# Kernel optimization log

Measured on AMD Instinct MI355X. Metric: run time of the kernel, lower is better.

The kernel has to match this reference:

```python
import jax, jax.numpy as jnp
import numpy as np

NEG_SLOPE = 0.2
K_L = 0.5
K_G = 0.5
TEMP_G = 1e-3


def _leaky(v):
    return jnp.where(v >= 0, v, NEG_SLOPE * v)


def _topk_row_mask(scores, keep):
    # scores: [n, n, h]; torch.topk(dim=0) -> indices [keep, n] per head,
    # then head_mask[indices, :] = 1 selects whole ROWS (any column hit).
    n = scores.shape[0]
    s = jnp.transpose(scores, (1, 2, 0))        # [n_cols, h, n_rows]
    _, idx = jax.lax.top_k(s, keep)             # [n_cols, h, keep]

    def per_head(idx_h):                        # idx_h: [n_cols, keep]
        return jnp.zeros((n,), scores.dtype).at[idx_h.reshape(-1)].set(1.0)

    rows = jax.vmap(per_head, in_axes=1, out_axes=0)(idx)  # [h, n_rows]
    return jnp.transpose(rows)[:, None, :]      # [n_rows, 1, h] broadcast over cols


def setup_inputs() -> dict:
    key = jax.random.key(0)
    ks = jax.random.split(key, 8)
    n, in_f, feat_dim = 1024, 256, 128
    H, F = 4, 64                                # n_heads, n_hidden (out_features=256)
    feats = jax.random.normal(ks[0], (n, feat_dim), dtype=jnp.float32)
    x = jax.random.normal(ks[1], (n, in_f), dtype=jnp.float32)
    adj = jax.random.randint(ks[2], (n, n, 1), 0, 2).astype(jnp.int32)
    sc = 0.05
    W_l = jax.random.normal(ks[3], (in_f, H * F), dtype=jnp.float32) * sc
    W_r = jax.random.normal(ks[4], (in_f, H * F), dtype=jnp.float32) * sc
    attn_w = jax.random.normal(ks[5], (F,), dtype=jnp.float32) * sc
    W_delta = jax.random.normal(ks[6], (2 * F, F), dtype=jnp.float32) * sc
    b_delta = jnp.zeros((F,), dtype=jnp.float32)
    return {"feats": feats, "x": x, "adj": adj, "W_l": W_l, "W_r": W_r,
            "attn_w": attn_w, "W_delta": W_delta, "b_delta": b_delta}


def reference(feats, x, adj, W_l, W_r, attn_w, W_delta, b_delta):
    n = x.shape[0]
    F = attn_w.shape[0]
    H = W_l.shape[1] // F
    g_l = (x @ W_l).reshape(n, H, F)
    g_r = (x @ W_r).reshape(n, H, F)
    # g_sum[i, j] = g_l[j] + g_r[i]  (repeat vs repeat_interleave ordering)
    g_sum = g_r[:, None, :, :] + g_l[None, :, :, :]          # [n, n, H, F]
    e = jnp.einsum('ijhf,f->ijh', _leaky(g_sum), attn_w)     # [n, n, H]

    mask_adj = adj > 0                                        # [n, n, 1]
    a_l = jax.nn.softmax(jnp.where(mask_adj, e, -jnp.inf), axis=1)
    a_1nd = a_l * mask_adj.astype(e.dtype)

    keep_l = int(n * (1.0 - K_L))
    a_filt = a_1nd * _topk_row_mask(a_1nd, keep_l)
    attn_local = jnp.einsum('ijh,jhf->ihf', a_filt, g_r)     # [n, H, F]

    omega = jax.nn.softmax(e, axis=1)
    fn = (feats - feats.min(axis=0)) / (feats.max(axis=0) - feats.min(axis=0))
    fn = jnp.where(jnp.isnan(fn), 0.0, fn)
    g_rn = (g_r - g_r.min(axis=0)) / (g_r.max(axis=0) - g_r.min(axis=0))
    nf = jnp.linalg.norm(fn, axis=1)                          # [n] (index j)
    ng = jnp.linalg.norm(g_rn, axis=2)                        # [n, H] (index i)
    alpha = jax.nn.softmax(jnp.abs(nf[None, :, None] - ng[:, None, :]), axis=1)
    gamma = 0.5 * (omega + (1.0 - alpha))

    keep_g = int(n * (1.0 - K_G))
    gf = gamma * _topk_row_mask(gamma, keep_g)
    gf = jax.nn.softmax(jnp.where(gf == 0, 1e-10, gf) / TEMP_G, axis=1)
    attn_global = jnp.einsum('ijh,jhf->ihf', gf, g_r)         # [n, H, F]

    inter = _leaky(jnp.concatenate([attn_local, attn_global], axis=2) @ W_delta + b_delta)
    delta = jax.nn.softmax(inter, axis=1)                     # softmax over heads (torch dim=1)
    attn_res = delta * attn_local + (1.0 - delta) * attn_global
    return attn_res.reshape(n, H * F)
```

## Files before the change

### kernel.cpp

```cpp
#include <hip/hip_runtime.h>
#include <cstdint>
#include <cstddef>

#define N 1024
#define HN 4
#define FDIM 64
#define KSEL 512
#define FLT_MAX_ 3.402823466e+38f

__device__ __forceinline__ float wred_sum(float v){
#pragma unroll
  for(int o=32;o>0;o>>=1) v += __shfl_down(v,o,64);
  return v;
}
__device__ __forceinline__ float bfly_sum(float v){
#pragma unroll
  for(int o=1;o<64;o<<=1) v += __shfl_xor(v,o,64);
  return v;
}
__device__ __forceinline__ float bfly_max(float v){
#pragma unroll
  for(int o=1;o<64;o<<=1) v = fmaxf(v,__shfl_xor(v,o,64));
  return v;
}
__device__ __forceinline__ int bfly_sumi(int v){
#pragma unroll
  for(int o=1;o<64;o<<=1) v += __shfl_xor(v,o,64);
  return v;
}
__device__ __forceinline__ float bred_sum(float v, float* scr){
  int t=threadIdx.x;
  v = wred_sum(v);
  __syncthreads();
  if((t&63)==0) scr[t>>6]=v;
  __syncthreads();
  return (scr[0]+scr[1])+(scr[2]+scr[3]);
}

__global__ __launch_bounds__(256) void stage1(const float* __restrict__ x,
                                              const float* __restrict__ W_l,
                                              const float* __restrict__ W_r,
                                              const int* __restrict__ adj,
                                              const float* __restrict__ feats,
                                              float* __restrict__ g_l,
                                              float* __restrict__ g_r,
                                              unsigned* __restrict__ adjbit,
                                              int* __restrict__ masks,
                                              float* __restrict__ pmin_f,
                                              float* __restrict__ pmax_f){
  int bx = blockIdx.x, t = threadIdx.x;
  if(bx < 512){
    const float* __restrict__ W = (bx >= 256) ? W_r : W_l;
    float* __restrict__ g = (bx >= 256) ? g_r : g_l;
    int i0 = (bx & 255)*4;
    float acc[4] = {0.f,0.f,0.f,0.f};
#pragma unroll 8
    for(int k=0;k<256;k++){
      float w = W[(size_t)k*256 + t];
#pragma unroll
      for(int r=0;r<4;r++) acc[r] = fmaf(x[(size_t)(i0+r)*256 + k], w, acc[r]);
    }
#pragma unroll
    for(int r=0;r<4;r++) g[(size_t)(i0+r)*256 + t] = acc[r];
  } else if(bx < 1536){
    int i = bx - 512, w = t>>6, lane = t&63;
    if(i < 32) masks[i*256 + t] = 0;
#pragma unroll
    for(int it=0; it<4; it++){
      int j = w*256 + it*64 + lane;
      int v = adj[(size_t)i*N + j];
      unsigned long long mb = __ballot(v > 0);
      if(lane == 0){
        adjbit[i*32 + w*8 + it*2]     = (unsigned)mb;
        adjbit[i*32 + w*8 + it*2 + 1] = (unsigned)(mb >> 32);
      }
    }
  } else {
    int chunk = bx - 1536;
    if(t < 128){
      float lo = FLT_MAX_, hi = -FLT_MAX_;
      int r0 = chunk*64;
      for(int r=0;r<64;r++){
        float v = feats[(size_t)(r0+r)*128 + t];
        lo = fminf(lo,v); hi = fmaxf(hi,v);
      }
      pmin_f[chunk*128+t]=lo; pmax_f[chunk*128+t]=hi;
    }
  }
}

__global__ __launch_bounds__(256) void stage2(const float* __restrict__ g_l,
                                              const float* __restrict__ g_r,
                                              const float* __restrict__ attn_w,
                                              const float* __restrict__ feats,
                                              const float* __restrict__ pmin_f, const float* __restrict__ pmax_f,
                                              float* __restrict__ pmin_g, float* __restrict__ pmax_g,
                                              float* __restrict__ nf,
                                              float* __restrict__ e){
  __shared__ __align__(16) float smem[2*64*68 + 128];
  int bx = blockIdx.x, t = threadIdx.x;
  if(bx < 1024){
    float* grs = smem;
    float* gls = smem + 64*68;
    float* aw  = smem + 2*64*68;
    float* aw2 = aw + 64;
    int h = bx >> 8, i0 = ((bx>>4)&15)*64, j0 = (bx&15)*64;
    if(t < 64){ float w = attn_w[t]; aw[t]=w; aw2[t]=0.2f*w; }
#pragma unroll
    for(int k=0;k<16;k++){
      int idx = t + k*256; int r = idx>>6, f = idx&63;
      grs[r*68+f] = g_r[(size_t)(i0+r)*256 + h*64 + f];
      gls[r*68+f] = g_l[(size_t)(j0+r)*256 + h*64 + f];
    }
    __syncthreads();
    int tj = t&15, ti = t>>4;
    float acc[4][4];
#pragma unroll
    for(int a=0;a<4;a++)
#pragma unroll
      for(int b=0;b<4;b++) acc[a][b]=0.f;
    for(int fc=0; fc<64; fc+=4){
      float4 wv  = *(float4*)&aw[fc];
      float4 wv2 = *(float4*)&aw2[fc];
      float4 ga4[4], gb4[4];
#pragma unroll
      for(int a=0;a<4;a++) ga4[a] = *(float4*)&grs[(ti*4+a)*68+fc];
#pragma unroll
      for(int b=0;b<4;b++) gb4[b] = *(float4*)&gls[(tj+16*b)*68+fc];
#pragma unroll
      for(int a=0;a<4;a++)
#pragma unroll
        for(int b=0;b<4;b++){
          float s0 = ga4[a].x + gb4[b].x;
          float s1 = ga4[a].y + gb4[b].y;
          float s2 = ga4[a].z + gb4[b].z;
          float s3 = ga4[a].w + gb4[b].w;
          acc[a][b] = fmaf(s0, (s0>=0.f)?wv.x:wv2.x, acc[a][b]);
          acc[a][b] = fmaf(s1, (s1>=0.f)?wv.y:wv2.y, acc[a][b]);
          acc[a][b] = fmaf(s2, (s2>=0.f)?wv.z:wv2.z, acc[a][b]);
          acc[a][b] = fmaf(s3, (s3>=0.f)?wv.w:wv2.w, acc[a][b]);
        }
    }
#pragma unroll
    for(int a=0;a<4;a++)
#pragma unroll
      for(int b=0;b<4;b++){
        int i = i0 + ti*4 + a, j = j0 + tj + 16*b;
        e[((size_t)h*N + i)*N + j] = acc[a][b];
      }
  } else if(bx < 1040){
    int chunk = bx - 1024;
    float lo = FLT_MAX_, hi = -FLT_MAX_;
    int r0 = chunk*64;
    for(int r=0;r<64;r++){
      float v = g_r[(size_t)(r0+r)*256 + t];
      lo = fminf(lo,v); hi = fmaxf(hi,v);
    }
    pmin_g[chunk*256+t]=lo; pmax_g[chunk*256+t]=hi;
  } else {
    int i = bx - 1040;
    float* scr = smem;
    float u = 0.f;
    if(t < 128){
      float lo = FLT_MAX_, hi = -FLT_MAX_;
#pragma unroll
      for(int k=0;k<16;k++){
        lo = fminf(lo, pmin_f[k*128+t]);
        hi = fmaxf(hi, pmax_f[k*128+t]);
      }
      float d = hi - lo;
      float v = feats[(size_t)i*128 + t];
      u = (d==0.f) ? 0.f : (v - lo)/d;
    }
    float tot = bred_sum(u*u, scr);
    if(t==0) nf[i] = sqrtf(tot);
  }
}

__global__ __launch_bounds__(256) void row_stats(const float* __restrict__ e,
                                                 const unsigned* __restrict__ adjbit,
                                                 const float* __restrict__ nf,
                                                 const float* __restrict__ g_r,
                                                 const float* __restrict__ pmin_g, const float* __restrict__ pmax_g,
                                                 float* __restrict__ ng,
                                                 float* __restrict__ mlA, float* __restrict__ islA,
                                                 float* __restrict__ moA, float* __restrict__ isoA,
                                                 float* __restrict__ maA, float* __restrict__ isaA,
                                                 float* __restrict__ mgA, float* __restrict__ sgA){
  int i = blockIdx.x, t = threadIdx.x, h = t>>6, lane = t&63;
  float glo = FLT_MAX_, ghi = -FLT_MAX_;
#pragma unroll
  for(int k=0;k<16;k++){
    glo = fminf(glo, pmin_g[k*256 + h*64 + lane]);
    ghi = fmaxf(ghi, pmax_g[k*256 + h*64 + lane]);
  }
  float dg = ghi - glo;
  float ug = (g_r[(size_t)i*256 + h*64 + lane] - glo)/dg;
  float ngv = sqrtf(bfly_sum(ug*ug));
  if(lane==0) ng[h*N + i] = ngv;

  size_t base = ((size_t)h*N + i)*N;
  float er[16], nfr[16];
  unsigned nib[4];
#pragma unroll
  for(int c=0;c<4;c++){
    float4 e4 = *(const float4*)(e  + base + c*256 + lane*4);
    float4 n4 = *(const float4*)(nf + c*256 + lane*4);
    er[c*4+0]=e4.x; er[c*4+1]=e4.y; er[c*4+2]=e4.z; er[c*4+3]=e4.w;
    nfr[c*4+0]=n4.x; nfr[c*4+1]=n4.y; nfr[c*4+2]=n4.z; nfr[c*4+3]=n4.w;
    nib[c] = (adjbit[i*32 + c*8 + (lane>>3)] >> ((lane&7)*4)) & 0xFu;
  }
  float ml=-FLT_MAX_, mo=-FLT_MAX_, ma=-FLT_MAX_;
#pragma unroll
  for(int c=0;c<4;c++)
#pragma unroll
    for(int k=0;k<4;k++){
      int q = c*4+k;
      float ev = er[q];
      mo = fmaxf(mo, ev);
      if((nib[c]>>k)&1) ml = fmaxf(ml, ev);
      ma = fmaxf(ma, fabsf(nfr[q]-ngv));
    }
  ml = bfly_max(ml); mo = bfly_max(mo); ma = bfly_max(ma);
  float sl=0.f, so=0.f, sa=0.f;
#pragma unroll
  for(int c=0;c<4;c++)
#pragma unroll
    for(int k=0;k<4;k++){
      int q = c*4+k;
      float ev = er[q];
      so += __expf(ev-mo);
      if((nib[c]>>k)&1) sl += __expf(ev-ml);
      sa += __expf(fabsf(nfr[q]-ngv)-ma);
    }
  sl = bfly_sum(sl); so = bfly_sum(so); sa = bfly_sum(sa);
  float isl = 1.f/sl, iso = 1.f/so, isa = 1.f/sa;
  float gg[16];
  float mg = -FLT_MAX_;
#pragma unroll
  for(int q=0;q<16;q++){
    float ev = er[q];
    float omega = __expf(ev-mo)*iso;
    float alpha = __expf(fabsf(nfr[q]-ngv)-ma)*isa;
    float g = 0.5f*(omega + 1.f - alpha);
    gg[q] = g;
    mg = fmaxf(mg, g);
  }
  mg = bfly_max(mg);
  float sg = 0.f;
#pragma unroll
  for(int q=0;q<16;q++) sg += __expf((gg[q]-mg)/1e-3f);
  sg = bfly_sum(sg);
  if(lane==0){
    mlA[h*N+i]=ml; islA[h*N+i]=isl;
    moA[h*N+i]=mo; isoA[h*N+i]=iso;
    maA[h*N+i]=ma; isaA[h*N+i]=isa;
    mgA[h*N+i]=mg; sgA[h*N+i]=sg;
  }
}

__global__ __launch_bounds__(256) void applyT(float* __restrict__ e,
                                              float* __restrict__ gamT,
                                              const unsigned* __restrict__ adjbit,
                                              const float* __restrict__ nf,
                                              const float* __restrict__ mlA, const float* __restrict__ islA,
                                              const float* __restrict__ moA, const float* __restrict__ isoA,
                                              const float* __restrict__ maA, const float* __restrict__ isaA,
                                              const float* __restrict__ ng){
  __shared__ __align__(16) float buf1[64][65];
  __shared__ __align__(16) float buf2[64][65];
  __shared__ __align__(16) float buf3[64][65];
  __shared__ float rml[64], risl[64], rmo[64], riso[64], rma[64], risa[64], rng[64], nfs[64];
  int h = blockIdx.y;
  int pp = blockIdx.x; int a = 0;
  while(pp >= 16 - a){ pp -= 16 - a; a++; }
  int b = a + pp;
  int t = threadIdx.x;
  int rg = t >> 4, c4 = t & 15;

  int i0 = a*64, j0 = b*64;
  if(t < 64){
    int o = h*N + i0 + t;
    rml[t]=mlA[o]; risl[t]=islA[o]; rmo[t]=moA[o]; riso[t]=isoA[o];
    rma[t]=maA[o]; risa[t]=isaA[o]; rng[t]=ng[o]; nfs[t]=nf[j0+t];
  }
  __syncthreads();
  float4 ev[4]; unsigned nb[4];
#pragma unroll
  for(int k=0;k<4;k++){
    int row = rg*4+k;
    ev[k] = *(const float4*)(e + ((size_t)h*N + i0+row)*N + j0 + c4*4);
    nb[k] = (adjbit[(size_t)(i0+row)*32 + (j0>>5) + (c4>>3)] >> ((c4&7)*4)) & 0xFu;
  }
#pragma unroll
  for(int k=0;k<4;k++){
    int row = rg*4+k;
    float ml=rml[row], isl=risl[row], mo=rmo[row], iso=riso[row];
    float ma=rma[row], isa=risa[row], ngv=rng[row];
    float evc[4] = {ev[k].x,ev[k].y,ev[k].z,ev[k].w};
#pragma unroll
    for(int c=0;c<4;c++){
      int j = c4*4+c;
      buf2[j][row] = ((nb[k]>>c)&1) ? __expf(evc[c]-ml)*isl : 0.f;
      float omega = __expf(evc[c]-mo)*iso;
      float alpha = __expf(fabsf(nfs[j]-ngv)-ma)*isa;
      buf1[j][row] = 0.5f*(omega + 1.f - alpha);
    }
  }
  __syncthreads();
#pragma unroll
  for(int k=0;k<4;k++){
    int jr = rg*4+k;
    *(float4*)(gamT + ((size_t)h*N + j0+jr)*N + i0 + c4*4) = *(float4*)&buf1[jr][c4*4];
  }
  if(a == b){
#pragma unroll
    for(int k=0;k<4;k++){
      int jr = rg*4+k;
      *(float4*)(e + ((size_t)h*N + j0+jr)*N + i0 + c4*4) = *(float4*)&buf2[jr][c4*4];
    }
    return;
  }
  int i1 = b*64, j1 = a*64;
  __syncthreads();
  if(t < 64){
    int o = h*N + i1 + t;
    rml[t]=mlA[o]; risl[t]=islA[o]; rmo[t]=moA[o]; riso[t]=isoA[o];
    rma[t]=maA[o]; risa[t]=isaA[o]; rng[t]=ng[o]; nfs[t]=nf[j1+t];
  }
#pragma unroll
  for(int k=0;k<4;k++){
    int row = rg*4+k;
    ev[k] = *(const float4*)(e + ((size_t)h*N + i1+row)*N + j1 + c4*4);
    nb[k] = (adjbit[(size_t)(i1+row)*32 + (j1>>5) + (c4>>3)] >> ((c4&7)*4)) & 0xFu;
  }
  __syncthreads();
#pragma unroll
  for(int k=0;k<4;k++){
    int jr = rg*4+k;
    *(float4*)(e + ((size_t)h*N + i1+jr)*N + j1 + c4*4) = *(float4*)&buf2[jr][c4*4];
  }
#pragma unroll
  for(int k=0;k<4;k++){
    int row = rg*4+k;
    float ml=rml[row], isl=risl[row], mo=rmo[row], iso=riso[row];
    float ma=rma[row], isa=risa[row], ngv=rng[row];
    float evc[4] = {ev[k].x,ev[k].y,ev[k].z,ev[k].w};
#pragma unroll
    for(int c=0;c<4;c++){
      int j = c4*4+c;
      buf3[j][row] = ((nb[k]>>c)&1) ? __expf(evc[c]-ml)*isl : 0.f;
      float omega = __expf(evc[c]-mo)*iso;
      float alpha = __expf(fabsf(nfs[j]-ngv)-ma)*isa;
      buf1[j][row] = 0.5f*(omega + 1.f - alpha);
    }
  }
  __syncthreads();
#pragma unroll
  for(int k=0;k<4;k++){
    int jr = rg*4+k;
    *(float4*)(gamT + ((size_t)h*N + j1+jr)*N + i1 + c4*4) = *(float4*)&buf1[jr][c4*4];
    *(float4*)(e    + ((size_t)h*N + j1+jr)*N + i1 + c4*4) = *(float4*)&buf3[jr][c4*4];
  }
}

__global__ __launch_bounds__(256) void colselect6(const float* __restrict__ a1T,
                                                  const float* __restrict__ gaT,
                                                  int* __restrict__ mask_l,
                                                  int* __restrict__ mask_g){
  __shared__ __align__(16) int hist[4][256];
  int t = threadIdx.x, w = t>>6, lane = t&63;
  int gcol = blockIdx.x*4 + w;
  int z  = gcol >> 12;
  int hj = gcol & 4095;
  int h  = hj >> 10;
  const float* __restrict__ src = (z ? gaT : a1T) + (size_t)hj * (size_t)N;
  int* __restrict__ mask = z ? mask_g : mask_l;
  int* hw = hist[w];

  unsigned ur[16];
#pragma unroll
  for(int c=0;c<4;c++){
    uint4 u4 = ((const uint4*)src)[c*64 + lane];
    ur[c*4+0]=u4.x; ur[c*4+1]=u4.y; ur[c*4+2]=u4.z; ur[c*4+3]=u4.w;
  }
  int np = 0;
#pragma unroll
  for(int q=0;q<16;q++) np += (ur[q] != 0u) ? 1 : 0;
  int cnt_pos = bfly_sumi(np);

  unsigned T; int tneed; int tiecnt = -1;
  if(cnt_pos < KSEL){
    T = 0u; tneed = KSEL - cnt_pos;
  } else {
    unsigned prefix = 0; int kth = KSEL;
#pragma unroll
    for(int b=3;b>=0;b--){
      *(int4*)&hw[lane*4] = make_int4(0,0,0,0);
#pragma unroll
      for(int q=0;q<16;q++){
        unsigned u = ur[q];
        bool act = (b==3) || ((u >> (8*(b+1))) == prefix);
        if(act){
          int bucket = (u >> (8*b)) & 0xFF;
          unsigned long long mball = __ballot(true);
          int lead = __ffsll(mball) - 1;
          int maj = __shfl(bucket, lead, 64);
          if(bucket == maj){
            int cnt = (int)__popcll(__ballot(true));
            if(lane == lead) atomicAdd(&hw[maj], cnt);
          } else {
            atomicAdd(&hw[bucket], 1);
          }
        }
      }
      int4 hv = *(int4*)&hw[lane*4];
      int s = hv.x+hv.y+hv.z+hv.w;
      int P = s;
#pragma unroll
      for(int off=1; off<64; off<<=1){
        int q2 = __shfl_up(P, off, 64);
        if(lane >= off) P += q2;
      }
      int total = __shfl(P, 63, 64);
      int suffChunk  = total - (P - s);
      int suffChunkN = total - P;
      bool cross = (suffChunk >= kth) && (suffChunkN < kth);
      int selb=0, newk=0, tcnt=0;
      if(cross){
        int s3 = suffChunkN + hv.w;
        int s2 = s3 + hv.z;
        int s1 = s2 + hv.y;
        if(s3 >= kth){ selb=4*lane+3; newk = kth - suffChunkN; tcnt=hv.w; }
        else if(s2 >= kth){ selb=4*lane+2; newk = kth - s3; tcnt=hv.z; }
        else if(s1 >= kth){ selb=4*lane+1; newk = kth - s2; tcnt=hv.y; }
        else { selb=4*lane; newk = kth - s1; tcnt=hv.x; }
      }
      unsigned long long cm = __ballot(cross);
      int csrc = __ffsll(cm) - 1;
      selb   = __shfl(selb, csrc, 64);
      kth    = __shfl(newk, csrc, 64);
      tiecnt = __shfl(tcnt, csrc, 64);
      prefix = (prefix << 8) | (unsigned)selb;
    }
    T = prefix; tneed = kth;
  }

  if(tiecnt == tneed){
#pragma unroll
    for(int c=0;c<4;c++)
#pragma unroll
      for(int k2=0;k2<4;k2++){
        int i = c*256 + lane*4 + k2;
        if(ur[c*4+k2] >= T) mask[h*N + i] = 1;
      }
  } else {
    int base = 0;
#pragma unroll
    for(int c=0;c<4;c++){
      int tc=0;
#pragma unroll
      for(int k2=0;k2<4;k2++) tc += (ur[c*4+k2]==T)?1:0;
      int pc = tc;
#pragma unroll
      for(int off=1; off<64; off<<=1){
        int q2 = __shfl_up(pc, off, 64);
        if(lane >= off) pc += q2;
      }
      int ctot = __shfl(pc, 63, 64);
      int run = base + pc - tc;
#pragma unroll
      for(int k2=0;k2<4;k2++){
        int i = c*256 + lane*4 + k2;
        unsigned u = ur[c*4+k2];
        bool sel = (u > T) || (u == T && run < tneed);
        run += (u==T)?1:0;
        if(sel) mask[h*N + i] = 1;
      }
      base += ctot;
    }
  }
}

__global__ __launch_bounds__(256) void attn_mm(const float* __restrict__ a1T,
                                               const float* __restrict__ gaT,
                                               const float* __restrict__ g_r,
                                               const float* __restrict__ mgA,
                                               const float* __restrict__ sgA,
                                               const int* __restrict__ mask_g,
                                               float* __restrict__ partL,
                                               float* __restrict__ partG){
  __shared__ __align__(16) float a_t[32][36];
  __shared__ __align__(16) float p_t[32][36];
  __shared__ __align__(16) float b_s[32][68];
  __shared__ float mgv[32], isgv[32];
  __shared__ int mgf[32];
  int i0 = blockIdx.x*32, h = blockIdx.y, s = blockIdx.z, j0 = s*128;
  int t = threadIdx.x;
  if(t < 32){
    mgv[t]  = mgA[h*N + i0 + t];
    isgv[t] = 1.f / sgA[h*N + i0 + t];
    mgf[t]  = mask_g[h*N + i0 + t];
  }
  __syncthreads();
  int fq = t & 15, iq = t >> 4;
  float4 accL[2], accG[2];
#pragma unroll
  for(int r=0;r<2;r++){ accL[r]=make_float4(0,0,0,0); accG[r]=make_float4(0,0,0,0); }
  for(int sub=0; sub<4; sub++){
    int jb = j0 + sub*32;
    {
      int jj = t>>3, i4 = t&7;
      size_t base = ((size_t)h*N + jb + jj)*N + i0 + i4*4;
      *(float4*)&a_t[jj][i4*4] = *(const float4*)(a1T + base);
      float4 g4 = *(const float4*)(gaT + base);
      int ii = i4*4;
      const float inv = 1.f/1024.f;
      float4 p4;
      p4.x = mgf[ii+0] ? __expf((g4.x - mgv[ii+0])/1e-3f)*isgv[ii+0] : inv;
      p4.y = mgf[ii+1] ? __expf((g4.y - mgv[ii+1])/1e-3f)*isgv[ii+1] : inv;
      p4.z = mgf[ii+2] ? __expf((g4.z - mgv[ii+2])/1e-3f)*isgv[ii+2] : inv;
      p4.w = mgf[ii+3] ? __expf((g4.w - mgv[ii+3])/1e-3f)*isgv[ii+3] : inv;
      *(float4*)&p_t[jj][i4*4] = p4;
#pragma unroll
      for(int k=0;k<2;k++){
        int idx = t + k*256;
        int jb2 = idx>>4, d4 = idx&15;
        *(float4*)&b_s[jb2][d4*4] = *(const float4*)(g_r + (size_t)(jb+jb2)*256 + h*64 + d4*4);
      }
    }
    __syncthreads();
#pragma unroll 8
    for(int j=0;j<32;j++){
      float4 bv = *(float4*)&b_s[j][fq*4];
      float2 av = *(float2*)&a_t[j][iq*2];
      float2 pv = *(float2*)&p_t[j][iq*2];
      accL[0].x = fmaf(av.x, bv.x, accL[0].x); accL[0].y = fmaf(av.x, bv.y, accL[0].y);
      accL[0].z = fmaf(av.x, bv.z, accL[0].z); accL[0].w = fmaf(av.x, bv.w, accL[0].w);
      accL[1].x = fmaf(av.y, bv.x, accL[1].x); accL[1].y = fmaf(av.y, bv.y, accL[1].y);
      accL[1].z = fmaf(av.y, bv.z, accL[1].z); accL[1].w = fmaf(av.y, bv.w, accL[1].w);
      accG[0].x = fmaf(pv.x, bv.x, accG[0].x); accG[0].y = fmaf(pv.x, bv.y, accG[0].y);
      accG[0].z = fmaf(pv.x, bv.z, accG[0].z); accG[0].w = fmaf(pv.x, bv.w, accG[0].w);
      accG[1].x = fmaf(pv.y, bv.x, accG[1].x); accG[1].y = fmaf(pv.y, bv.y, accG[1].y);
      accG[1].z = fmaf(pv.y, bv.z, accG[1].z); accG[1].w = fmaf(pv.y, bv.w, accG[1].w);
    }
    __syncthreads();
  }
#pragma unroll
  for(int r=0;r<2;r++){
    int i = i0 + iq*2 + r;
    size_t o = ((size_t)s*N + i)*256 + h*64 + fq*4;
    *(float4*)&partL[o] = accL[r];
    *(float4*)&partG[o] = accG[r];
  }
}

__global__ __launch_bounds__(256) void epilogue(const float* __restrict__ partL,
                                                const float* __restrict__ partG,
                                                const int* __restrict__ mask_l,
                                                const float* __restrict__ W_delta,
                                                const float* __restrict__ b_delta,
                                                float* __restrict__ out){
  __shared__ float cat[4][128];
  __shared__ float inter_s[4][64];
  int i = blockIdx.x, t = threadIdx.x;
  int h = t>>6, f = t&63;
  float sl = 0.f, sg = 0.f;
#pragma unroll
  for(int s2=0;s2<8;s2++){
    size_t o = ((size_t)s2*N + i)*256 + h*64 + f;
    sl += partL[o];
    sg += partG[o];
  }
  if(!mask_l[h*N + i]) sl = 0.f;
  cat[h][f]      = sl;
  cat[h][64 + f] = sg;
  __syncthreads();
  float d = b_delta[f];
  for(int c=0;c<128;c++) d = fmaf(cat[h][c], W_delta[(size_t)c*64 + f], d);
  d = (d >= 0.f) ? d : 0.2f*d;
  inter_s[h][f] = d;
  __syncthreads();
  float m = inter_s[0][f];
#pragma unroll
  for(int hh=1;hh<4;hh++) m = fmaxf(m, inter_s[hh][f]);
  float ssum = 0.f;
#pragma unroll
  for(int hh=0;hh<4;hh++) ssum += __expf(inter_s[hh][f]-m);
  float delta = __expf(d - m)/ssum;
  out[(size_t)i*256 + h*64 + f] = delta*sl + (1.f - delta)*sg;
}

extern "C" void kernel_launch(void* const* d_in, const int* in_sizes, int n_in,
                              void* d_out, int out_size, void* d_ws, size_t ws_size,
                              hipStream_t stream) {
  const float* feats  = (const float*)d_in[0];
  const float* x      = (const float*)d_in[1];
  const int*   adj    = (const int*)  d_in[2];
  const float* W_l    = (const float*)d_in[3];
  const float* W_r    = (const float*)d_in[4];
  const float* attn_w = (const float*)d_in[5];
  const float* W_delta= (const float*)d_in[6];
  const float* b_delta= (const float*)d_in[7];
  float* out = (float*)d_out;

  float* ws = (float*)d_ws;
  size_t off = 0;
  float* g_l   = ws+off; off += (size_t)N*256;
  float* g_r   = ws+off; off += (size_t)N*256;
  float* e     = ws+off; off += (size_t)HN*N*N;
  float* gam   = ws+off; off += (size_t)HN*N*N;
  float* partL = ws+off; off += (size_t)8*N*256;
  float* partG = ws+off; off += (size_t)8*N*256;
  float* pmin_f= ws+off; off += 16*128;
  float* pmax_f= ws+off; off += 16*128;
  float* pmin_g= ws+off; off += 16*256;
  float* pmax_g= ws+off; off += 16*256;
  float* nf    = ws+off; off += N;
  float* ng    = ws+off; off += (size_t)HN*N;
  float* mlA   = ws+off; off += (size_t)HN*N;
  float* islA  = ws+off; off += (size_t)HN*N;
  float* moA   = ws+off; off += (size_t)HN*N;
  float* isoA  = ws+off; off += (size_t)HN*N;
  float* maA   = ws+off; off += (size_t)HN*N;
  float* isaA  = ws+off; off += (size_t)HN*N;
  float* mgA   = ws+off; off += (size_t)HN*N;
  float* sgA   = ws+off; off += (size_t)HN*N;
  int* mask_l  = (int*)(ws+off); off += (size_t)HN*N;
  int* mask_g  = (int*)(ws+off); off += (size_t)HN*N;
  unsigned* adjbit = (unsigned*)(ws+off); off += (size_t)N*32;

  stage1<<<1552, 256, 0, stream>>>(x, W_l, W_r, adj, feats, g_l, g_r, adjbit, mask_l, pmin_f, pmax_f);

  stage2<<<2064, 256, 0, stream>>>(g_l, g_r, attn_w, feats, pmin_f, pmax_f,
                                   pmin_g, pmax_g, nf, e);

  row_stats<<<N, 256, 0, stream>>>(e, adjbit, nf, g_r, pmin_g, pmax_g, ng,
                                   mlA, islA, moA, isoA, maA, isaA, mgA, sgA);

  applyT<<<dim3(136,HN), 256, 0, stream>>>(e, gam, adjbit, nf, mlA, islA, moA, isoA, maA, isaA, ng);

  colselect6<<<2048, 256, 0, stream>>>(e, gam, mask_l, mask_g);

  attn_mm<<<dim3(32,HN,8), 256, 0, stream>>>(e, gam, g_r, mgA, sgA, mask_g, partL, partG);

  epilogue<<<N, 256, 0, stream>>>(partL, partG, mask_l, W_delta, b_delta, out);
}
```

Before: 195.2 us.

## Double-buffer attn_mm LDS tiles and widen block tile to 64 rows

The attn_mm kernel now tiles 64 output rows per block instead of 32, so each thread accumulates a 4x4 register tile rather than 2x4, which halves the grid. Shared-memory tiles are double-buffered: global loads for the next 32-column chunk go into registers while the current chunk is computed, then are written to the other buffer. The aim is to hide global load latency and raise FMA work per LDS read. The cost is more registers and shared memory per block and fewer blocks (512) to spread across CUs.

```diff
diff --git a/kernel.cpp b/kernel.cpp
--- a/kernel.cpp
+++ b/kernel.cpp
@@ -490,65 +490,106 @@
                                                const int* __restrict__ mask_g,
                                                float* __restrict__ partL,
                                                float* __restrict__ partG){
-  __shared__ __align__(16) float a_t[32][36];
-  __shared__ __align__(16) float p_t[32][36];
-  __shared__ __align__(16) float b_s[32][68];
-  __shared__ float mgv[32], isgv[32];
-  __shared__ int mgf[32];
-  int i0 = blockIdx.x*32, h = blockIdx.y, s = blockIdx.z, j0 = s*128;
+  __shared__ __align__(16) float a_t[2][32][68];
+  __shared__ __align__(16) float p_t[2][32][68];
+  __shared__ __align__(16) float b_s[2][32][68];
+  __shared__ float mgv[64], isgv[64];
+  __shared__ int mgf[64];
+  int i0 = blockIdx.x*64, h = blockIdx.y, s = blockIdx.z, j0 = s*128;
   int t = threadIdx.x;
-  if(t < 32){
+  if(t < 64){
     mgv[t]  = mgA[h*N + i0 + t];
     isgv[t] = 1.f / sgA[h*N + i0 + t];
     mgf[t]  = mask_g[h*N + i0 + t];
   }
-  __syncthreads();
   int fq = t & 15, iq = t >> 4;
-  float4 accL[2], accG[2];
-#pragma unroll
-  for(int r=0;r<2;r++){ accL[r]=make_float4(0,0,0,0); accG[r]=make_float4(0,0,0,0); }
-  for(int sub=0; sub<4; sub++){
-    int jb = j0 + sub*32;
-    {
-      int jj = t>>3, i4 = t&7;
-      size_t base = ((size_t)h*N + jb + jj)*N + i0 + i4*4;
-      *(float4*)&a_t[jj][i4*4] = *(const float4*)(a1T + base);
-      float4 g4 = *(const float4*)(gaT + base);
-      int ii = i4*4;
-      const float inv = 1.f/1024.f;
-      float4 p4;
+  int ju0 = t>>4,        i40 = t&15;
+  int ju1 = (t+256)>>4,  i41 = t&15;
+
+  float4 va[2], vg[2], vb[2];
+  {
+    int jb = j0;
+    size_t b0 = ((size_t)h*N + jb + ju0)*N + i0 + i40*4;
+    size_t b1 = ((size_t)h*N + jb + ju1)*N + i0 + i41*4;
+    va[0] = *(const float4*)(a1T + b0);  va[1] = *(const float4*)(a1T + b1);
+    vg[0] = *(const float4*)(gaT + b0);  vg[1] = *(const float4*)(gaT + b1);
+    vb[0] = *(const float4*)(g_r + (size_t)(jb+ju0)*256 + h*64 + i40*4);
+    vb[1] = *(const float4*)(g_r + (size_t)(jb+ju1)*256 + h*64 + i41*4);
+  }
+  __syncthreads();
+  {
+    const float inv = 1.f/1024.f;
+#pragma unroll
+    for(int k=0;k<2;k++){
+      int ju = k ? ju1 : ju0, ii = (k ? i41 : i40)*4;
+      *(float4*)&a_t[0][ju][(k?i41:i40)*4] = va[k];
+      float4 g4 = vg[k], p4;
       p4.x = mgf[ii+0] ? __expf((g4.x - mgv[ii+0])/1e-3f)*isgv[ii+0] : inv;
       p4.y = mgf[ii+1] ? __expf((g4.y - mgv[ii+1])/1e-3f)*isgv[ii+1] : inv;
       p4.z = mgf[ii+2] ? __expf((g4.z - mgv[ii+2])/1e-3f)*isgv[ii+2] : inv;
       p4.w = mgf[ii+3] ? __expf((g4.w - mgv[ii+3])/1e-3f)*isgv[ii+3] : inv;
-      *(float4*)&p_t[jj][i4*4] = p4;
-#pragma unroll
-      for(int k=0;k<2;k++){
-        int idx = t + k*256;
-        int jb2 = idx>>4, d4 = idx&15;
-        *(float4*)&b_s[jb2][d4*4] = *(const float4*)(g_r + (size_t)(jb+jb2)*256 + h*64 + d4*4);
-      }
-    }
+      *(float4*)&p_t[0][ju][(k?i41:i40)*4] = p4;
+      *(float4*)&b_s[0][ju][(k?i41:i40)*4] = vb[k];
+    }
+  }
+  float4 accL[4], accG[4];
+#pragma unroll
+  for(int r=0;r<4;r++){ accL[r]=make_float4(0,0,0,0); accG[r]=make_float4(0,0,0,0); }
+
+  for(int sub=0; sub<4; sub++){
+    int cur = sub & 1;
     __syncthreads();
-#pragma unroll 8
+    if(sub < 3){
+      int jb = j0 + (sub+1)*32;
+      size_t b0 = ((size_t)h*N + jb + ju0)*N + i0 + i40*4;
+      size_t b1 = ((size_t)h*N + jb + ju1)*N + i0 + i41*4;
+      va[0] = *(const float4*)(a1T + b0);  va[1] = *(const float4*)(a1T + b1);
+      vg[0] = *(const float4*)(gaT + b0);  vg[1] = *(const float4*)(gaT + b1);
+      vb[0] = *(const float4*)(g_r + (size_t)(jb+ju0)*256 + h*64 + i40*4);
+      vb[1] = *(const float4*)(g_r + (size_t)(jb+ju1)*256 + h*64 + i41*4);
+    }
+#pragma unroll 4
     for(int j=0;j<32;j++){
-      float4 bv = *(float4*)&b_s[j][fq*4];
-      float2 av = *(float2*)&a_t[j][iq*2];
-      float2 pv = *(float2*)&p_t[j][iq*2];
+      float4 bv = *(float4*)&b_s[cur][j][fq*4];
+      float4 av = *(float4*)&a_t[cur][j][iq*4];
+      float4 pv = *(float4*)&p_t[cur][j][iq*4];
       accL[0].x = fmaf(av.x, bv.x, accL[0].x); accL[0].y = fmaf(av.x, bv.y, accL[0].y);
       accL[0].z = fmaf(av.x, bv.z, accL[0].z); accL[0].w = fmaf(av.x, bv.w, accL[0].w);
       accL[1].x = fmaf(av.y, bv.x, accL[1].x); accL[1].y = fmaf(av.y, bv.y, accL[1].y);
       accL[1].z = fmaf(av.y, bv.z, accL[1].z); accL[1].w = fmaf(av.y, bv.w, accL[1].w);
+      accL[2].x = fmaf(av.z, bv.x, accL[2].x); accL[2].y = fmaf(av.z, bv.y, accL[2].y);
+      accL[2].z = fmaf(av.z, bv.z, accL[2].z); accL[2].w = fmaf(av.z, bv.w, accL[2].w);
+      accL[3].x = fmaf(av.w, bv.x, accL[3].x); accL[3].y = fmaf(av.w, bv.y, accL[3].y);
+      accL[3].z = fmaf(av.w, bv.z, accL[3].z); accL[3].w = fmaf(av.w, bv.w, accL[3].w);
       accG[0].x = fmaf(pv.x, bv.x, accG[0].x); accG[0].y = fmaf(pv.x, bv.y, accG[0].y);
       accG[0].z = fmaf(pv.x, bv.z, accG[0].z); accG[0].w = fmaf(pv.x, bv.w, accG[0].w);
       accG[1].x = fmaf(pv.y, bv.x, accG[1].x); accG[1].y = fmaf(pv.y, bv.y, accG[1].y);
       accG[1].z = fmaf(pv.y, bv.z, accG[1].z); accG[1].w = fmaf(pv.y, bv.w, accG[1].w);
-    }
-    __syncthreads();
-  }
-#pragma unroll
-  for(int r=0;r<2;r++){
-    int i = i0 + iq*2 + r;
+      accG[2].x = fmaf(pv.z, bv.x, accG[2].x); accG[2].y = fmaf(pv.z, bv.y, accG[2].y);
+      accG[2].z = fmaf(pv.z, bv.z, accG[2].z); accG[2].w = fmaf(pv.z, bv.w, accG[2].w);
+      accG[3].x = fmaf(pv.w, bv.x, accG[3].x); accG[3].y = fmaf(pv.w, bv.y, accG[3].y);
+      accG[3].z = fmaf(pv.w, bv.z, accG[3].z); accG[3].w = fmaf(pv.w, bv.w, accG[3].w);
+    }
+    if(sub < 3){
+      int nxt = 1 - cur;
+      const float inv = 1.f/1024.f;
+#pragma unroll
+      for(int k=0;k<2;k++){
+        int ju = k ? ju1 : ju0, ii = (k ? i41 : i40)*4;
+        *(float4*)&a_t[nxt][ju][(k?i41:i40)*4] = va[k];
+        float4 g4 = vg[k], p4;
+        p4.x = mgf[ii+0] ? __expf((g4.x - mgv[ii+0])/1e-3f)*isgv[ii+0] : inv;
+        p4.y = mgf[ii+1] ? __expf((g4.y - mgv[ii+1])/1e-3f)*isgv[ii+1] : inv;
+        p4.z = mgf[ii+2] ? __expf((g4.z - mgv[ii+2])/1e-3f)*isgv[ii+2] : inv;
+        p4.w = mgf[ii+3] ? __expf((g4.w - mgv[ii+3])/1e-3f)*isgv[ii+3] : inv;
+        *(float4*)&p_t[nxt][ju][(k?i41:i40)*4] = p4;
+        *(float4*)&b_s[nxt][ju][(k?i41:i40)*4] = vb[k];
+      }
+    }
+  }
+#pragma unroll
+  for(int r=0;r<4;r++){
+    int i = i0 + iq*4 + r;
     size_t o = ((size_t)s*N + i)*256 + h*64 + fq*4;
     *(float4*)&partL[o] = accL[r];
     *(float4*)&partG[o] = accG[r];
@@ -642,7 +683,7 @@
 
   colselect6<<<2048, 256, 0, stream>>>(e, gam, mask_l, mask_g);
 
-  attn_mm<<<dim3(32,HN,8), 256, 0, stream>>>(e, gam, g_r, mgA, sgA, mask_g, partL, partG);
+  attn_mm<<<dim3(16,HN,8), 256, 0, stream>>>(e, gam, g_r, mgA, sgA, mask_g, partL, partG);
 
   epilogue<<<N, 256, 0, stream>>>(partL, partG, mask_l, W_delta, b_delta, out);
 }
```

Result: no change. 196.1 us (+0.4%).
